# Kernel tuning notes

Hardware: AMD Instinct MI355X
Metric: run time of the kernel (lower is better)

## Reference

```python
import jax, jax.numpy as jnp
import numpy as np

D_MODEL = 1024
NHEAD = 16
NUM_KV = 4
D_K = D_MODEL // NHEAD          # 64
GROUP = NHEAD // NUM_KV          # 4 query heads per kv head
ROPE_BASE = 10000.0


def _rope(x, seq_len):
    """Apply rotary embedding. x: [B, h, S, d_k], positions 0..seq_len-1."""
    half = D_K // 2
    inv_freq = 1.0 / (ROPE_BASE ** (jnp.arange(0, D_K, 2, dtype=jnp.float32) / D_K))
    t = jnp.arange(seq_len, dtype=jnp.float32)
    freqs = jnp.outer(t, inv_freq)                      # [S, d_k/2]
    emb = jnp.concatenate([freqs, freqs], axis=-1)      # [S, d_k]
    cos, sin = jnp.cos(emb), jnp.sin(emb)               # broadcast over B, h
    x1, x2 = x[..., :half], x[..., half:]
    rot = jnp.concatenate([-x2, x1], axis=-1)
    return x * cos + rot * sin


def setup_inputs() -> dict:
    key = jax.random.key(0)
    ks = jax.random.split(key, 12)
    B, S = 2, 2048
    s_in = 1.0 / np.sqrt(D_MODEL)
    inp = {
        "query": jax.random.normal(ks[0], (B, S, D_MODEL), jnp.float32),
        "key":   jax.random.normal(ks[1], (B, S, D_MODEL), jnp.float32),
        "value": jax.random.normal(ks[2], (B, S, D_MODEL), jnp.float32),
        "Wq": jax.random.normal(ks[3], (D_MODEL, D_MODEL), jnp.float32) * s_in,
        "bq": jnp.zeros((D_MODEL,), jnp.float32),
        "Wk": jax.random.normal(ks[4], (NUM_KV * D_K, D_MODEL), jnp.float32) * s_in,
        "bk": jnp.zeros((NUM_KV * D_K,), jnp.float32),
        "Wv": jax.random.normal(ks[5], (NUM_KV * D_K, D_MODEL), jnp.float32) * s_in,
        "bv": jnp.zeros((NUM_KV * D_K,), jnp.float32),
        "Wo": jax.random.normal(ks[6], (D_MODEL, D_MODEL), jnp.float32) * s_in,
        "bo": jnp.zeros((D_MODEL,), jnp.float32),
    }
    return inp


def reference(query, key, value, Wq, bq, Wk, bk, Wv, bv, Wo, bo):
    B, S, _ = query.shape
    T = key.shape[1]
    # projections (torch Linear: x @ W^T + b)
    Q = (query @ Wq.T + bq).reshape(B, S, NHEAD, D_K).transpose(0, 2, 1, 3)   # [B,H,S,dk]
    K = (key   @ Wk.T + bk).reshape(B, T, NUM_KV, D_K).transpose(0, 2, 1, 3)  # [B,KV,T,dk]
    V = (value @ Wv.T + bv).reshape(B, T, NUM_KV, D_K).transpose(0, 2, 1, 3)
    # fused RoPE (start_pos = 0)
    Q = _rope(Q, S)
    K = _rope(K, T)
    # expand kv heads (repeat_interleave on head dim)
    Kr = jnp.repeat(K, GROUP, axis=1)   # [B,H,T,dk]
    Vr = jnp.repeat(V, GROUP, axis=1)
    scale = 1.0 / np.sqrt(D_K)
    scores = jnp.einsum("bhsd,bhtd->bhst", Q, Kr) * scale   # [B,H,S,T]
    attn = jax.nn.softmax(scores, axis=-1)                    # dropout = eval/no-op
    context = jnp.einsum("bhst,bhtd->bhsd", attn, Vr)        # [B,H,S,dk]
    context = context.transpose(0, 2, 1, 3).reshape(B, S, D_MODEL)
    return context @ Wo.T + bo
```

## Files before the change

kernel.cpp:

```cpp
#include <hip/hip_runtime.h>
#include <hip/hip_bf16.h>

typedef __hip_bfloat16 bf16;
typedef __attribute__((ext_vector_type(8))) short short8;
typedef __attribute__((ext_vector_type(4))) short short4v;
typedef __attribute__((ext_vector_type(4))) float f32x4;
typedef __attribute__((ext_vector_type(4))) float float4v;

static __device__ inline short f2bf(float f){
  __hip_bfloat16 h = __float2bfloat16(f);
  return *reinterpret_cast<short*>(&h);
}

static __device__ __forceinline__ unsigned cvt_pk_bf16(float lo, float hi){
  unsigned r;
  asm("v_cvt_pk_bf16_f32 %0, %1, %2" : "=v"(r) : "v"(lo), "v"(hi));
  return r;
}

static __device__ __forceinline__ float exp2_fast(float x){
  float r;
  asm("v_exp_f32 %0, %1" : "=v"(r) : "v"(x));
  return r;
}

static __device__ __forceinline__ float max3f(float a, float b, float c){
  float r;
  asm("v_max3_f32 %0, %1, %2, %3" : "=v"(r) : "v"(a), "v"(b), "v"(c));
  return r;
}

static __device__ inline short8 load8(const float* p){
  float4v a = *reinterpret_cast<const float4v*>(p);
  float4v b = *reinterpret_cast<const float4v*>(p + 4);
  short8 r;
  unsigned* u = reinterpret_cast<unsigned*>(&r);
  u[0] = cvt_pk_bf16(a[0], a[1]);
  u[1] = cvt_pk_bf16(a[2], a[3]);
  u[2] = cvt_pk_bf16(b[0], b[1]);
  u[3] = cvt_pk_bf16(b[2], b[3]);
  return r;
}
static __device__ inline short8 load8(const bf16* p){
  return *reinterpret_cast<const short8*>(p);
}

typedef __attribute__((address_space(1))) const unsigned int gas_u32;
typedef __attribute__((address_space(3))) unsigned int las_u32;
static __device__ __forceinline__ void gload16(const void* g, void* l){
  __builtin_amdgcn_global_load_lds((gas_u32*)g, (las_u32*)l, 16, 0, 0);
}

template<int N>
static __device__ __forceinline__ void vm_barrier(){
  if constexpr (N == 8) asm volatile("s_waitcnt vmcnt(8)" ::: "memory");
  else if constexpr (N == 4) asm volatile("s_waitcnt vmcnt(4)" ::: "memory");
  else if constexpr (N == 2) asm volatile("s_waitcnt vmcnt(2)" ::: "memory");
  else asm volatile("s_waitcnt vmcnt(0)" ::: "memory");
  __builtin_amdgcn_s_barrier();
  __builtin_amdgcn_sched_barrier(0);
}

#define CVT_Q   0
#define CVT_K   4194304
#define CVT_V   8388608
#define CVT_WQ  12582912
#define CVT_WK  13631488
#define CVT_WV  13893632
#define CVT_WO  14155776
#define CVT_TOT 15204352
__global__ void cvt_kernel(bf16* __restrict__ dst, float* __restrict__ tab,
    const float* q, const float* k, const float* v,
    const float* wq, const float* wk, const float* wv, const float* wo){
  if (blockIdx.x < 256){
    const int idx = blockIdx.x * 256 + threadIdx.x;
    const int d = idx & 31, s = idx >> 5;
    const float ang = (float)s * exp2f(-0.41524101186092030f * (float)d);
    float sn, cs;
    sincosf(ang, &sn, &cs);
    tab[idx*2] = cs; tab[idx*2+1] = sn;
  }
  const size_t i8 = ((size_t)blockIdx.x * 256 + threadIdx.x) * 8;
  const float* src; size_t off;
  if      (i8 < CVT_K ){ src = q;  off = i8; }
  else if (i8 < CVT_V ){ src = k;  off = i8 - CVT_K; }
  else if (i8 < CVT_WQ){ src = v;  off = i8 - CVT_V; }
  else if (i8 < CVT_WK){ src = wq; off = i8 - CVT_WQ; }
  else if (i8 < CVT_WV){ src = wk; off = i8 - CVT_WK; }
  else if (i8 < CVT_WO){ src = wv; off = i8 - CVT_WV; }
  else                 { src = wo; off = i8 - CVT_WO; }
  *reinterpret_cast<short8*>(reinterpret_cast<short*>(dst) + i8) = load8(src + off);
}

template<int MODE>
__device__ __forceinline__ void gemm_bt_v2(
    short* lds, void* __restrict__ Cout,
    const bf16* __restrict__ A, const bf16* __restrict__ B,
    const float* __restrict__ bias, const float* __restrict__ tab,
    int ntile, int mtile, int N, int K)
{
  const int NK = K >> 5;
  const int n0 = ntile * 128, m0 = mtile * 128;
  const int tid = threadIdx.x, w = tid >> 6, lane = tid & 63;
  const int wm = w >> 1, wn = w & 1, lr = lane & 15, lg = lane >> 4;
  const int r0 = w*32 + (lane >> 2), r1 = r0 + 16;
  const int c0 = ((lane & 3) ^ ((r0 >> 1) & 3)) * 8;
  const int c1 = ((lane & 3) ^ ((r1 >> 1) & 3)) * 8;
  const bf16* A0 = A + (size_t)(m0 + r0) * K + c0;
  const bf16* A1 = A + (size_t)(m0 + r1) * K + c1;
  const bf16* B0 = B + (size_t)(n0 + r0) * K + c0;
  const bf16* B1 = B + (size_t)(n0 + r1) * K + c1;
  const int ldsW = (w*32) * 32;
  int offA[4], offB[4];
  #pragma unroll
  for (int i = 0; i < 4; i++){
    const int ra = wm*64 + i*16 + lr;
    offA[i] = ra*64 + ((lg ^ ((ra >> 1) & 3)) * 16);
    const int rb = wn*64 + i*16 + lr;
    offB[i] = rb*64 + ((lg ^ ((rb >> 1) & 3)) * 16);
  }
  auto stage = [&](int t){
    short* bufA = lds + (t & 3) * 8192;
    short* bufB = bufA + 4096;
    gload16(A0 + t*32, bufA + ldsW);
    gload16(A1 + t*32, bufA + ldsW + 512);
    gload16(B0 + t*32, bufB + ldsW);
    gload16(B1 + t*32, bufB + ldsW + 512);
  };
  f32x4 acc[4][4] = {};
  stage(0); stage(1);
  for (int t = 0; t < NK; t++){
    if (t + 2 < NK){ stage(t + 2); vm_barrier<8>(); }
    else if (t + 1 < NK){ vm_barrier<4>(); }
    else { vm_barrier<0>(); }
    const char* bufA = (const char*)(lds + (t & 3) * 8192);
    const char* bufB = bufA + 8192;
    short8 af[4], bfm[4];
    #pragma unroll
    for (int mt = 0; mt < 4; mt++) af[mt]  = *(const short8*)(bufA + offA[mt]);
    #pragma unroll
    for (int nt = 0; nt < 4; nt++) bfm[nt] = *(const short8*)(bufB + offB[nt]);
    __builtin_amdgcn_s_setprio(1);
    #pragma unroll
    for (int mt = 0; mt < 4; mt++)
      #pragma unroll
      for (int nt = 0; nt < 4; nt++)
        acc[mt][nt] = __builtin_amdgcn_mfma_f32_16x16x32_bf16(af[mt], bfm[nt], acc[mt][nt], 0, 0, 0);
    __builtin_amdgcn_s_setprio(0);
  }
  if constexpr (MODE == 0){
    float* C = (float*)Cout;
    #pragma unroll
    for (int mt = 0; mt < 4; mt++){
      #pragma unroll
      for (int nt = 0; nt < 4; nt++){
        const int col = n0 + wn*64 + nt*16 + lr;
        const float bv = bias[col];
        const int rbase = m0 + wm*64 + mt*16 + lg*4;
        #pragma unroll
        for (int i = 0; i < 4; i++)
          C[(size_t)(rbase + i) * N + col] = acc[mt][nt][i] + bv;
      }
    }
  } else if constexpr (MODE == 1 || MODE == 2){
    bf16* dst = (bf16*)Cout;
    constexpr int NH = (MODE == 1) ? 16 : 4;
    constexpr float SC = (MODE == 1) ? 0.18033688011112042f : 1.0f;
    #pragma unroll
    for (int mt = 0; mt < 4; mt++){
      #pragma unroll
      for (int nt = 0; nt < 2; nt++){
        const int col = n0 + wn*64 + nt*16 + lr;
        const int d = col & 63;
        const int hh = col >> 6;
        const float b1 = bias[col], b2 = bias[col + 32];
        #pragma unroll
        for (int i = 0; i < 4; i++){
          const int m = m0 + wm*64 + mt*16 + lg*4 + i;
          const int s = m & 2047, bb = m >> 11;
          const float cs = tab[(s*32 + d)*2], sn = tab[(s*32 + d)*2 + 1];
          const float x1 = acc[mt][nt][i] + b1;
          const float x2 = acc[mt][nt+2][i] + b2;
          const size_t o = ((size_t)(bb*NH + hh) * 2048 + s) * 64 + d;
          dst[o]      = __float2bfloat16((x1*cs - x2*sn) * SC);
          dst[o + 32] = __float2bfloat16((x2*cs + x1*sn) * SC);
        }
      }
    }
  } else {
    bf16* dst = (bf16*)Cout;
    #pragma unroll
    for (int mt = 0; mt < 4; mt++){
      #pragma unroll
      for (int nt = 0; nt < 4; nt++){
        const int col = n0 + wn*64 + nt*16 + lr;
        const int kv = col >> 6, d = col & 63;
        const float bv = bias[col];
        #pragma unroll
        for (int i = 0; i < 4; i++){
          const int m = m0 + wm*64 + mt*16 + lg*4 + i;
          const int s = m & 2047, bb = m >> 11;
          dst[((size_t)(bb*4 + kv) * 64 + d) * 2048 + s] = __float2bfloat16(acc[mt][nt][i] + bv);
        }
      }
    }
  }
}

__global__ __launch_bounds__(256, 2) void gemm_qkv_kernel(
    bf16* Qa, bf16* Ka, bf16* Va, const bf16* cvt,
    const float* bq, const float* bk, const float* bv, const float* tab){
  __shared__ short lds[4 * 8192];
  const int pid = blockIdx.x;
  const int x = pid >> 5;
  const int y = (pid & 7) * 4 + ((pid >> 3) & 3);
  if (x < 8)
    gemm_bt_v2<1>(lds, Qa, cvt + CVT_Q, cvt + CVT_WQ, bq, tab, x,    y, 1024, 1024);
  else if (x < 10)
    gemm_bt_v2<2>(lds, Ka, cvt + CVT_K, cvt + CVT_WK, bk, tab, x-8,  y, 256, 1024);
  else
    gemm_bt_v2<3>(lds, Va, cvt + CVT_V, cvt + CVT_WV, bv, tab, x-10, y, 256, 1024);
}
__global__ __launch_bounds__(256, 2) void gemm_out_kernel(
    float* C, const bf16* ctx, const bf16* cvt, const float* bo){
  __shared__ short lds[4 * 8192];
  const int pid = blockIdx.x;
  const int x = pid >> 5;
  const int y = (pid & 7) * 4 + ((pid >> 3) & 3);
  gemm_bt_v2<0>(lds, C, ctx, cvt + CVT_WO, bo, nullptr, x, y, 1024, 1024);
}

__global__ __launch_bounds__(256, 2) void attn_kernel(
    bf16* __restrict__ ctx, const bf16* __restrict__ Qa,
    const bf16* __restrict__ Ka, const bf16* __restrict__ Vt)
{
  __shared__ short Klds[4][64 * 64];
  __shared__ short Vlds[4][64 * 64];
  const int pid = blockIdx.y * 16 + blockIdx.x;
  const int bh = (pid & 7) * 4 + ((pid >> 3) & 3);
  const int q0 = (pid >> 5) * 128;
  const int b = bh >> 4, h = bh & 15, kvh = h >> 2;
  const int tid = threadIdx.x, w = tid >> 6, lane = tid & 63;
  const int lr = lane & 15, lg = lane >> 4;
  const bf16* Qbase = Qa + (size_t)bh * 2048 * 64;
  const bf16* Kbase = Ka + (size_t)(b*4 + kvh) * 2048 * 64;
  const bf16* Vbase = Vt + (size_t)(b*4 + kvh) * 64 * 2048;

  short8 qf[2][2];
  #pragma unroll
  for (int qt = 0; qt < 2; qt++){
    qf[qt][0] = load8(Qbase + (size_t)(q0 + w*32 + qt*16 + lr) * 64 + lg*8);
    qf[qt][1] = load8(Qbase + (size_t)(q0 + w*32 + qt*16 + lr) * 64 + 32 + lg*8);
  }

  const int xsw = (lr & 7) << 4;
  const int koff0 = lr*128 + ((lg*16) ^ xsw);
  const int koff1 = lr*128 + ((64 + lg*16) ^ xsw);
  int voff[2][2];
  #pragma unroll
  for (int kkA = 0; kkA < 2; kkA++)
    #pragma unroll
    for (int hh = 0; hh < 2; hh++)
      voff[kkA][hh] = lr*128 + ((kkA*64 + lg*8 + hh*32) ^ xsw);

  const int l8 = lane >> 3;
  const int ch = (lane & 7) ^ l8;
  const bf16* kSrc = Kbase + (size_t)(w*16 + l8) * 64 + ch*8;
  const bf16* vSrc = Vbase + (size_t)(w*16 + l8) * 2048 + ch*8;
  auto stage = [&](int bi, int t){
    short* Kd = &Klds[bi][(w*16) * 64];
    short* Vd = &Vlds[bi][(w*16) * 64];
    const bf16* ks = kSrc + (size_t)t * 64 * 64;
    const bf16* vs = vSrc + t * 64;
    gload16(ks,           Kd);
    gload16(ks + 8*64,    Kd + 8*64);
    gload16(vs,           Vd);
    gload16(vs + 8*2048,  Vd + 8*64);
  };

  float mrow[2] = {-1e30f, -1e30f};
  f32x4 o[2][4] = {};
  f32x4 acc_l[2] = {};
  short8 ones;
  #pragma unroll
  for (int j = 0; j < 4; j++) reinterpret_cast<unsigned*>(&ones)[j] = 0x3F803F80u;

  auto qk = [&](const char* Kc, f32x4 (&st)[4][2]){
    __builtin_amdgcn_s_setprio(1);
    #pragma unroll
    for (int mt = 0; mt < 4; mt++){
      short8 kf0 = *reinterpret_cast<const short8*>(Kc + mt*2048 + koff0);
      short8 kf1 = *reinterpret_cast<const short8*>(Kc + mt*2048 + koff1);
      #pragma unroll
      for (int qt = 0; qt < 2; qt++){
        st[mt][qt] = __builtin_amdgcn_mfma_f32_16x16x32_bf16(kf0, qf[qt][0], (f32x4){0.f,0.f,0.f,0.f}, 0, 0, 0);
        st[mt][qt] = __builtin_amdgcn_mfma_f32_16x16x32_bf16(kf1, qf[qt][1], st[mt][qt], 0, 0, 0);
      }
    }
    __builtin_amdgcn_s_setprio(0);
  };

  auto softmax_pv = [&](f32x4 (&st)[4][2], const char* Vc){
    short8 pf[2][2];
    #pragma unroll
    for (int qt = 0; qt < 2; qt++){
      const float m0 = max3f(st[0][qt][0], st[0][qt][1], st[0][qt][2]);
      const float m1 = max3f(st[0][qt][3], st[1][qt][0], st[1][qt][1]);
      const float m2 = max3f(st[1][qt][2], st[1][qt][3], st[2][qt][0]);
      const float m3 = max3f(st[2][qt][1], st[2][qt][2], st[2][qt][3]);
      const float m4 = max3f(st[3][qt][0], st[3][qt][1], st[3][qt][2]);
      float mx = fmaxf(max3f(m0, m1, m2), max3f(m3, m4, st[3][qt][3]));
      if (__any(mx > mrow[qt] + 8.0f)){
        mx = fmaxf(mx, __shfl_xor(mx, 16));
        mx = fmaxf(mx, __shfl_xor(mx, 32));
        const float nm = fmaxf(mrow[qt], mx);
        const float alpha = exp2_fast(mrow[qt] - nm);
        mrow[qt] = nm;
        float ab[4];
        #pragma unroll
        for (int i = 0; i < 4; i++) ab[i] = __shfl(alpha, lg*4 + i);
        #pragma unroll
        for (int dt = 0; dt < 4; dt++)
          #pragma unroll
          for (int i = 0; i < 4; i++)
            o[qt][dt][i] *= ab[i];
        #pragma unroll
        for (int i = 0; i < 4; i++) acc_l[qt][i] *= ab[i];
      }
      unsigned* pw = reinterpret_cast<unsigned*>(&pf[qt][0]);
      #pragma unroll
      for (int j = 0; j < 8; j++){
        const int mt = j >> 1, i0 = (j & 1) * 2;
        const float e0 = exp2_fast(st[mt][qt][i0]     - mrow[qt]);
        const float e1 = exp2_fast(st[mt][qt][i0 + 1] - mrow[qt]);
        pw[j] = cvt_pk_bf16(e0, e1);
      }
    }
    __builtin_amdgcn_s_setprio(1);
    #pragma unroll
    for (int qt = 0; qt < 2; qt++){
      acc_l[qt] = __builtin_amdgcn_mfma_f32_16x16x32_bf16(pf[qt][0], ones, acc_l[qt], 0, 0, 0);
      acc_l[qt] = __builtin_amdgcn_mfma_f32_16x16x32_bf16(pf[qt][1], ones, acc_l[qt], 0, 0, 0);
    }
    #pragma unroll
    for (int dt = 0; dt < 4; dt++){
      #pragma unroll
      for (int kkA = 0; kkA < 2; kkA++){
        short8 vf;
        *reinterpret_cast<short4v*>(&vf) =
            *reinterpret_cast<const short4v*>(Vc + dt*2048 + voff[kkA][0]);
        *reinterpret_cast<short4v*>(reinterpret_cast<short*>(&vf) + 4) =
            *reinterpret_cast<const short4v*>(Vc + dt*2048 + voff[kkA][1]);
        #pragma unroll
        for (int qt = 0; qt < 2; qt++)
          o[qt][dt] = __builtin_amdgcn_mfma_f32_16x16x32_bf16(pf[qt][kkA], vf, o[qt][dt], 0, 0, 0);
      }
    }
    __builtin_amdgcn_s_setprio(0);
  };

  f32x4 stA[4][2], stB[4][2];

  stage(0, 0); stage(1, 1);
  vm_barrier<4>();
  qk((const char*)&Klds[0][0], stA);

  for (int tt = 0; tt < 32; tt += 2){
    if (tt + 2 < 32){ stage((tt+2) & 3, tt+2); vm_barrier<4>(); }
    else vm_barrier<0>();
    qk((const char*)&Klds[(tt+1) & 3][0], stB);
    softmax_pv(stA, (const char*)&Vlds[tt & 3][0]);
    if (tt + 3 < 32){ stage((tt+3) & 3, tt+3); vm_barrier<4>(); }
    else vm_barrier<0>();
    if (tt + 2 < 32) qk((const char*)&Klds[(tt+2) & 3][0], stA);
    softmax_pv(stB, (const char*)&Vlds[(tt+1) & 3][0]);
  }

  #pragma unroll
  for (int qt = 0; qt < 2; qt++){
    float lb[4];
    #pragma unroll
    for (int i = 0; i < 4; i++) lb[i] = 1.0f / acc_l[qt][i];
    #pragma unroll
    for (int dt = 0; dt < 4; dt++){
      #pragma unroll
      for (int i = 0; i < 4; i++){
        const int q = q0 + w*32 + qt*16 + lg*4 + i;
        ctx[(size_t)(b*2048 + q) * 1024 + h*64 + dt*16 + lr] =
            __float2bfloat16(o[qt][dt][i] * lb[i]);
      }
    }
  }
}

extern "C" void kernel_launch(void* const* d_in, const int* in_sizes, int n_in,
                              void* d_out, int out_size, void* d_ws, size_t ws_size,
                              hipStream_t stream)
{
  const float* query = (const float*)d_in[0];
  const float* key   = (const float*)d_in[1];
  const float* value = (const float*)d_in[2];
  const float* Wq = (const float*)d_in[3];
  const float* bq = (const float*)d_in[4];
  const float* Wk = (const float*)d_in[5];
  const float* bk = (const float*)d_in[6];
  const float* Wv = (const float*)d_in[7];
  const float* bv = (const float*)d_in[8];
  const float* Wo = (const float*)d_in[9];
  const float* bo = (const float*)d_in[10];
  float* out = (float*)d_out;

  char* ws = (char*)d_ws;
  size_t off = 0;
  float* tab = (float*)(ws + off); off += (size_t)2048 * 32 * 2 * 4;
  bf16*  Qa  = (bf16*)(ws + off);  off += (size_t)32 * 2048 * 64 * 2;
  bf16*  Ka  = (bf16*)(ws + off);  off += (size_t)8 * 2048 * 64 * 2;
  bf16*  Va  = (bf16*)(ws + off);  off += (size_t)8 * 64 * 2048 * 2;
  bf16*  ctx = (bf16*)(ws + off);  off += (size_t)2 * 2048 * 1024 * 2;
  bf16*  cvt = (bf16*)(ws + off);  off += (size_t)CVT_TOT * 2;

  cvt_kernel<<<CVT_TOT / 8 / 256, 256, 0, stream>>>(cvt, tab, query, key, value, Wq, Wk, Wv, Wo);
  gemm_qkv_kernel<<<384, 256, 0, stream>>>(Qa, Ka, Va, cvt, bq, bk, bv, tab);
  attn_kernel<<<dim3(16, 32), 256, 0, stream>>>(ctx, Qa, Ka, Va);
  gemm_out_kernel<<<256, 256, 0, stream>>>(out, ctx, cvt, bo);
}
```

Measured before the change: 104.2 us.

## Use 128-key attention tiles with double-buffered LDS and a simple loop

The attention kernel now processes 128 keys per iteration instead of 64. It uses two LDS buffers with a new XOR-swizzled V layout, in place of a four-deep ring. The software-pipelined schedule that overlapped the next tile's QK with the current tile's softmax/PV is removed in favour of a straight loop: prefetch the next tile, compute, then barrier. This halves loop iterations and barrier count and amortises softmax bookkeeping over larger tiles. In exchange it gives up the intra-wave overlap of QK and softmax/PV and doubles the score registers held per wave, which may reduce latency hiding.

After: 100.4 us (median of 2 runs). 3.6% less time.

```diff
diff --git a/kernel.cpp b/kernel.cpp
--- a/kernel.cpp
+++ b/kernel.cpp
@@ -234,8 +234,8 @@
     bf16* __restrict__ ctx, const bf16* __restrict__ Qa,
     const bf16* __restrict__ Ka, const bf16* __restrict__ Vt)
 {
-  __shared__ short Klds[4][64 * 64];
-  __shared__ short Vlds[4][64 * 64];
+  __shared__ short Klds[2][128 * 64];
+  __shared__ short Vlds[2][64 * 128];
   const int pid = blockIdx.y * 16 + blockIdx.x;
   const int bh = (pid & 7) * 4 + ((pid >> 3) & 3);
   const int q0 = (pid >> 5) * 128;
@@ -253,29 +253,33 @@
     qf[qt][1] = load8(Qbase + (size_t)(q0 + w*32 + qt*16 + lr) * 64 + 32 + lg*8);
   }
 
-  const int xsw = (lr & 7) << 4;
-  const int koff0 = lr*128 + ((lg*16) ^ xsw);
-  const int koff1 = lr*128 + ((64 + lg*16) ^ xsw);
-  int voff[2][2];
-  #pragma unroll
-  for (int kkA = 0; kkA < 2; kkA++)
+  const int xswk = (lr & 7) << 4;
+  const int koff0 = lr*128 + ((lg*16) ^ xswk);
+  const int koff1 = lr*128 + ((64 + lg*16) ^ xswk);
+  int voff[4][2];
+  #pragma unroll
+  for (int kkA = 0; kkA < 4; kkA++)
     #pragma unroll
     for (int hh = 0; hh < 2; hh++)
-      voff[kkA][hh] = lr*128 + ((kkA*64 + lg*8 + hh*32) ^ xsw);
+      voff[kkA][hh] = lr*256 + (((kkA*4 + hh*2 + (lg >> 1)) ^ lr) << 4) + (lg & 1)*8;
 
   const int l8 = lane >> 3;
-  const int ch = (lane & 7) ^ l8;
-  const bf16* kSrc = Kbase + (size_t)(w*16 + l8) * 64 + ch*8;
-  const bf16* vSrc = Vbase + (size_t)(w*16 + l8) * 2048 + ch*8;
+  const int chk = (lane & 7) ^ l8;
+  const bf16* kSrc = Kbase + (size_t)(w*32 + l8) * 64 + chk*8;
+  const int vr0 = lane >> 4;
+  const bf16* vSrc[4];
+  #pragma unroll
+  for (int j = 0; j < 4; j++)
+    vSrc[j] = Vbase + (size_t)(w*16 + j*4 + vr0) * 2048 + ((lane & 15) ^ (j*4 + vr0)) * 8;
+
   auto stage = [&](int bi, int t){
-    short* Kd = &Klds[bi][(w*16) * 64];
-    short* Vd = &Vlds[bi][(w*16) * 64];
-    const bf16* ks = kSrc + (size_t)t * 64 * 64;
-    const bf16* vs = vSrc + t * 64;
-    gload16(ks,           Kd);
-    gload16(ks + 8*64,    Kd + 8*64);
-    gload16(vs,           Vd);
-    gload16(vs + 8*2048,  Vd + 8*64);
+    short* Kd = &Klds[bi][(w*32) * 64];
+    short* Vd = &Vlds[bi][(w*16) * 128];
+    const bf16* ks = kSrc + (size_t)t * 8192;
+    #pragma unroll
+    for (int j = 0; j < 4; j++) gload16(ks + j*512, Kd + j*512);
+    #pragma unroll
+    for (int j = 0; j < 4; j++) gload16(vSrc[j] + t*128, Vd + j*512);
   };
 
   float mrow[2] = {-1e30f, -1e30f};
@@ -285,10 +289,18 @@
   #pragma unroll
   for (int j = 0; j < 4; j++) reinterpret_cast<unsigned*>(&ones)[j] = 0x3F803F80u;
 
-  auto qk = [&](const char* Kc, f32x4 (&st)[4][2]){
+  f32x4 st[8][2];
+
+  stage(0, 0);
+  vm_barrier<0>();
+
+  for (int t = 0; t < 16; t++){
+    if (t + 1 < 16) stage((t+1) & 1, t+1);
+
+    const char* Kc = (const char*)&Klds[t & 1][0];
     __builtin_amdgcn_s_setprio(1);
     #pragma unroll
-    for (int mt = 0; mt < 4; mt++){
+    for (int mt = 0; mt < 8; mt++){
       short8 kf0 = *reinterpret_cast<const short8*>(Kc + mt*2048 + koff0);
       short8 kf1 = *reinterpret_cast<const short8*>(Kc + mt*2048 + koff1);
       #pragma unroll
@@ -298,18 +310,18 @@
       }
     }
     __builtin_amdgcn_s_setprio(0);
-  };
-
-  auto softmax_pv = [&](f32x4 (&st)[4][2], const char* Vc){
-    short8 pf[2][2];
+
+    short8 pf[2][4];
     #pragma unroll
     for (int qt = 0; qt < 2; qt++){
-      const float m0 = max3f(st[0][qt][0], st[0][qt][1], st[0][qt][2]);
-      const float m1 = max3f(st[0][qt][3], st[1][qt][0], st[1][qt][1]);
-      const float m2 = max3f(st[1][qt][2], st[1][qt][3], st[2][qt][0]);
-      const float m3 = max3f(st[2][qt][1], st[2][qt][2], st[2][qt][3]);
-      const float m4 = max3f(st[3][qt][0], st[3][qt][1], st[3][qt][2]);
-      float mx = fmaxf(max3f(m0, m1, m2), max3f(m3, m4, st[3][qt][3]));
+      float m8[8];
+      #pragma unroll
+      for (int mt = 0; mt < 8; mt++)
+        m8[mt] = fmaxf(max3f(st[mt][qt][0], st[mt][qt][1], st[mt][qt][2]), st[mt][qt][3]);
+      const float a  = max3f(m8[0], m8[1], m8[2]);
+      const float bb = max3f(m8[3], m8[4], m8[5]);
+      const float c  = max3f(m8[6], m8[7], a);
+      float mx = fmaxf(bb, c);
       if (__any(mx > mrow[qt] + 8.0f)){
         mx = fmaxf(mx, __shfl_xor(mx, 16));
         mx = fmaxf(mx, __shfl_xor(mx, 32));
@@ -329,51 +341,38 @@
       }
       unsigned* pw = reinterpret_cast<unsigned*>(&pf[qt][0]);
       #pragma unroll
-      for (int j = 0; j < 8; j++){
-        const int mt = j >> 1, i0 = (j & 1) * 2;
+      for (int p = 0; p < 16; p++){
+        const int mt = p >> 1, i0 = (p & 1) * 2;
         const float e0 = exp2_fast(st[mt][qt][i0]     - mrow[qt]);
         const float e1 = exp2_fast(st[mt][qt][i0 + 1] - mrow[qt]);
-        pw[j] = cvt_pk_bf16(e0, e1);
-      }
-    }
+        pw[p] = cvt_pk_bf16(e0, e1);
+      }
+    }
+
+    const char* Vc = (const char*)&Vlds[t & 1][0];
     __builtin_amdgcn_s_setprio(1);
     #pragma unroll
-    for (int qt = 0; qt < 2; qt++){
-      acc_l[qt] = __builtin_amdgcn_mfma_f32_16x16x32_bf16(pf[qt][0], ones, acc_l[qt], 0, 0, 0);
-      acc_l[qt] = __builtin_amdgcn_mfma_f32_16x16x32_bf16(pf[qt][1], ones, acc_l[qt], 0, 0, 0);
-    }
+    for (int qt = 0; qt < 2; qt++)
+      #pragma unroll
+      for (int kkA = 0; kkA < 4; kkA++)
+        acc_l[qt] = __builtin_amdgcn_mfma_f32_16x16x32_bf16(pf[qt][kkA], ones, acc_l[qt], 0, 0, 0);
     #pragma unroll
     for (int dt = 0; dt < 4; dt++){
       #pragma unroll
-      for (int kkA = 0; kkA < 2; kkA++){
+      for (int kkA = 0; kkA < 4; kkA++){
         short8 vf;
         *reinterpret_cast<short4v*>(&vf) =
-            *reinterpret_cast<const short4v*>(Vc + dt*2048 + voff[kkA][0]);
+            *reinterpret_cast<const short4v*>(Vc + dt*4096 + voff[kkA][0]);
         *reinterpret_cast<short4v*>(reinterpret_cast<short*>(&vf) + 4) =
-            *reinterpret_cast<const short4v*>(Vc + dt*2048 + voff[kkA][1]);
+            *reinterpret_cast<const short4v*>(Vc + dt*4096 + voff[kkA][1]);
         #pragma unroll
         for (int qt = 0; qt < 2; qt++)
           o[qt][dt] = __builtin_amdgcn_mfma_f32_16x16x32_bf16(pf[qt][kkA], vf, o[qt][dt], 0, 0, 0);
       }
     }
     __builtin_amdgcn_s_setprio(0);
-  };
-
-  f32x4 stA[4][2], stB[4][2];
-
-  stage(0, 0); stage(1, 1);
-  vm_barrier<4>();
-  qk((const char*)&Klds[0][0], stA);
-
-  for (int tt = 0; tt < 32; tt += 2){
-    if (tt + 2 < 32){ stage((tt+2) & 3, tt+2); vm_barrier<4>(); }
-    else vm_barrier<0>();
-    qk((const char*)&Klds[(tt+1) & 3][0], stB);
-    softmax_pv(stA, (const char*)&Vlds[tt & 3][0]);
-    if (tt + 3 < 32){ stage((tt+3) & 3, tt+3); vm_barrier<4>(); }
-    else vm_barrier<0>();
-    if (tt + 2 < 32) qk((const char*)&Klds[(tt+2) & 3][0], stA);
-    softmax_pv(stB, (const char*)&Vlds[(tt+1) & 3][0]);
+
+    if (t + 1 < 16) vm_barrier<0>();
   }
 
   #pragma unroll
```

## Split attention KV range across warps with LDS merge of partial softmax

Applied to the files above, without the earlier changes.

The attention kernel now gives each block 32 queries instead of 128, and each of its 4 warps walks a separate quarter of the 2048 keys. Every warp keeps its own private LDS slice with single-buffered staging. At the end the warps write their partial outputs, row maxima and row sums to LDS and merge them flash-decoding style. The grid grows from 512 to 2048 blocks to raise parallelism and occupancy, at the cost of 4x more Q-side block overhead, extra K/V global reads per query, and a final LDS reduction.

Measured after the change: 128.5 us, median of 2. 23.3% more time.

```diff
diff --git a/kernel.cpp b/kernel.cpp
--- a/kernel.cpp
+++ b/kernel.cpp
@@ -234,48 +234,48 @@
     bf16* __restrict__ ctx, const bf16* __restrict__ Qa,
     const bf16* __restrict__ Ka, const bf16* __restrict__ Vt)
 {
-  __shared__ short Klds[4][64 * 64];
-  __shared__ short Vlds[4][64 * 64];
-  const int pid = blockIdx.y * 16 + blockIdx.x;
+  __shared__ char lds[4][16384];
+  const int pid = blockIdx.x;
   const int bh = (pid & 7) * 4 + ((pid >> 3) & 3);
-  const int q0 = (pid >> 5) * 128;
+  const int q0 = (pid >> 5) * 32;
   const int b = bh >> 4, h = bh & 15, kvh = h >> 2;
   const int tid = threadIdx.x, w = tid >> 6, lane = tid & 63;
   const int lr = lane & 15, lg = lane >> 4;
   const bf16* Qbase = Qa + (size_t)bh * 2048 * 64;
   const bf16* Kbase = Ka + (size_t)(b*4 + kvh) * 2048 * 64;
   const bf16* Vbase = Vt + (size_t)(b*4 + kvh) * 64 * 2048;
+  char* Kc = lds[w];
+  char* Vc = lds[w] + 8192;
+  const int kv0 = w * 512;
 
   short8 qf[2][2];
   #pragma unroll
   for (int qt = 0; qt < 2; qt++){
-    qf[qt][0] = load8(Qbase + (size_t)(q0 + w*32 + qt*16 + lr) * 64 + lg*8);
-    qf[qt][1] = load8(Qbase + (size_t)(q0 + w*32 + qt*16 + lr) * 64 + 32 + lg*8);
-  }
-
-  const int xsw = (lr & 7) << 4;
-  const int koff0 = lr*128 + ((lg*16) ^ xsw);
-  const int koff1 = lr*128 + ((64 + lg*16) ^ xsw);
+    qf[qt][0] = load8(Qbase + (size_t)(q0 + qt*16 + lr) * 64 + lg*8);
+    qf[qt][1] = load8(Qbase + (size_t)(q0 + qt*16 + lr) * 64 + 32 + lg*8);
+  }
+
+  const int xs = lr & 7;
+  const int koff0 = lr*128 + ((lg       ^ xs) << 4);
+  const int koff1 = lr*128 + (((4 + lg) ^ xs) << 4);
   int voff[2][2];
   #pragma unroll
   for (int kkA = 0; kkA < 2; kkA++)
     #pragma unroll
     for (int hh = 0; hh < 2; hh++)
-      voff[kkA][hh] = lr*128 + ((kkA*64 + lg*8 + hh*32) ^ xsw);
+      voff[kkA][hh] = lr*128 + (((kkA*4 + hh*2 + (lg >> 1)) ^ xs) << 4) + (lg & 1)*8;
 
   const int l8 = lane >> 3;
   const int ch = (lane & 7) ^ l8;
-  const bf16* kSrc = Kbase + (size_t)(w*16 + l8) * 64 + ch*8;
-  const bf16* vSrc = Vbase + (size_t)(w*16 + l8) * 2048 + ch*8;
-  auto stage = [&](int bi, int t){
-    short* Kd = &Klds[bi][(w*16) * 64];
-    short* Vd = &Vlds[bi][(w*16) * 64];
-    const bf16* ks = kSrc + (size_t)t * 64 * 64;
-    const bf16* vs = vSrc + t * 64;
-    gload16(ks,           Kd);
-    gload16(ks + 8*64,    Kd + 8*64);
-    gload16(vs,           Vd);
-    gload16(vs + 8*2048,  Vd + 8*64);
+  const bf16* kS = Kbase + (size_t)(kv0 + l8) * 64 + ch*8;
+  const bf16* vS = Vbase + (size_t)l8 * 2048 + kv0 + ch*8;
+  auto stage = [&](int t){
+    const bf16* ks = kS + (size_t)t * 4096;
+    #pragma unroll
+    for (int jj = 0; jj < 8; jj++) gload16(ks + jj*512, Kc + jj*1024);
+    const bf16* vs = vS + t * 64;
+    #pragma unroll
+    for (int jj = 0; jj < 8; jj++) gload16(vs + (size_t)jj*16384, Vc + jj*1024);
   };
 
   float mrow[2] = {-1e30f, -1e30f};
@@ -285,7 +285,12 @@
   #pragma unroll
   for (int j = 0; j < 4; j++) reinterpret_cast<unsigned*>(&ones)[j] = 0x3F803F80u;
 
-  auto qk = [&](const char* Kc, f32x4 (&st)[4][2]){
+  stage(0);
+  asm volatile("s_waitcnt vmcnt(0)" ::: "memory");
+  __builtin_amdgcn_sched_barrier(0);
+
+  for (int t = 0; t < 8; t++){
+    f32x4 st[4][2];
     __builtin_amdgcn_s_setprio(1);
     #pragma unroll
     for (int mt = 0; mt < 4; mt++){
@@ -298,9 +303,21 @@
       }
     }
     __builtin_amdgcn_s_setprio(0);
-  };
-
-  auto softmax_pv = [&](f32x4 (&st)[4][2], const char* Vc){
+
+    short8 vf[4][2];
+    #pragma unroll
+    for (int dt = 0; dt < 4; dt++)
+      #pragma unroll
+      for (int kkA = 0; kkA < 2; kkA++){
+        *reinterpret_cast<short4v*>(&vf[dt][kkA]) =
+            *reinterpret_cast<const short4v*>(Vc + dt*2048 + voff[kkA][0]);
+        *reinterpret_cast<short4v*>(reinterpret_cast<short*>(&vf[dt][kkA]) + 4) =
+            *reinterpret_cast<const short4v*>(Vc + dt*2048 + voff[kkA][1]);
+      }
+    asm volatile("s_waitcnt lgkmcnt(0)" ::: "memory");
+    __builtin_amdgcn_sched_barrier(0);
+    if (t + 1 < 8) stage(t + 1);
+
     short8 pf[2][2];
     #pragma unroll
     for (int qt = 0; qt < 2; qt++){
@@ -336,6 +353,7 @@
         pw[j] = cvt_pk_bf16(e0, e1);
       }
     }
+
     __builtin_amdgcn_s_setprio(1);
     #pragma unroll
     for (int qt = 0; qt < 2; qt++){
@@ -343,51 +361,68 @@
       acc_l[qt] = __builtin_amdgcn_mfma_f32_16x16x32_bf16(pf[qt][1], ones, acc_l[qt], 0, 0, 0);
     }
     #pragma unroll
+    for (int dt = 0; dt < 4; dt++)
+      #pragma unroll
+      for (int kkA = 0; kkA < 2; kkA++)
+        #pragma unroll
+        for (int qt = 0; qt < 2; qt++)
+          o[qt][dt] = __builtin_amdgcn_mfma_f32_16x16x32_bf16(pf[qt][kkA], vf[dt][kkA], o[qt][dt], 0, 0, 0);
+    __builtin_amdgcn_s_setprio(0);
+
+    if (t + 1 < 8){
+      asm volatile("s_waitcnt vmcnt(0)" ::: "memory");
+      __builtin_amdgcn_sched_barrier(0);
+    }
+  }
+
+  float* Wf = (float*)lds[w];
+  #pragma unroll
+  for (int qt = 0; qt < 2; qt++){
+    #pragma unroll
+    for (int dt = 0; dt < 4; dt++)
+      #pragma unroll
+      for (int i = 0; i < 4; i++)
+        Wf[(qt*16 + lg*4 + i)*64 + dt*16 + lr] = o[qt][dt][i];
+    #pragma unroll
+    for (int i = 0; i < 4; i++){
+      const float mq = __shfl(mrow[qt], lg*4 + i);
+      if (lr == 0){
+        Wf[2048 + qt*32 + (lg*4 + i)*2]     = mq;
+        Wf[2048 + qt*32 + (lg*4 + i)*2 + 1] = acc_l[qt][i];
+      }
+    }
+  }
+  asm volatile("s_waitcnt lgkmcnt(0)" ::: "memory");
+  __builtin_amdgcn_s_barrier();
+  __builtin_amdgcn_sched_barrier(0);
+
+  #pragma unroll
+  for (int qt = 0; qt < 2; qt++){
+    float lbi[4], sc0[4], sc1[4], sc2[4], sc3[4];
+    #pragma unroll
+    for (int i = 0; i < 4; i++){
+      const int slot = 2048 + qt*32 + (lg*4 + i)*2;
+      const float mw0 = ((const float*)lds[0])[slot], lw0 = ((const float*)lds[0])[slot+1];
+      const float mw1 = ((const float*)lds[1])[slot], lw1 = ((const float*)lds[1])[slot+1];
+      const float mw2 = ((const float*)lds[2])[slot], lw2 = ((const float*)lds[2])[slot+1];
+      const float mw3 = ((const float*)lds[3])[slot], lw3 = ((const float*)lds[3])[slot+1];
+      const float M = fmaxf(max3f(mw0, mw1, mw2), mw3);
+      sc0[i] = exp2_fast(mw0 - M); sc1[i] = exp2_fast(mw1 - M);
+      sc2[i] = exp2_fast(mw2 - M); sc3[i] = exp2_fast(mw3 - M);
+      lbi[i] = 1.0f / (lw0*sc0[i] + lw1*sc1[i] + lw2*sc2[i] + lw3*sc3[i]);
+    }
+    #pragma unroll
     for (int dt = 0; dt < 4; dt++){
       #pragma unroll
-      for (int kkA = 0; kkA < 2; kkA++){
-        short8 vf;
-        *reinterpret_cast<short4v*>(&vf) =
-            *reinterpret_cast<const short4v*>(Vc + dt*2048 + voff[kkA][0]);
-        *reinterpret_cast<short4v*>(reinterpret_cast<short*>(&vf) + 4) =
-            *reinterpret_cast<const short4v*>(Vc + dt*2048 + voff[kkA][1]);
-        #pragma unroll
-        for (int qt = 0; qt < 2; qt++)
-          o[qt][dt] = __builtin_amdgcn_mfma_f32_16x16x32_bf16(pf[qt][kkA], vf, o[qt][dt], 0, 0, 0);
-      }
-    }
-    __builtin_amdgcn_s_setprio(0);
-  };
-
-  f32x4 stA[4][2], stB[4][2];
-
-  stage(0, 0); stage(1, 1);
-  vm_barrier<4>();
-  qk((const char*)&Klds[0][0], stA);
-
-  for (int tt = 0; tt < 32; tt += 2){
-    if (tt + 2 < 32){ stage((tt+2) & 3, tt+2); vm_barrier<4>(); }
-    else vm_barrier<0>();
-    qk((const char*)&Klds[(tt+1) & 3][0], stB);
-    softmax_pv(stA, (const char*)&Vlds[tt & 3][0]);
-    if (tt + 3 < 32){ stage((tt+3) & 3, tt+3); vm_barrier<4>(); }
-    else vm_barrier<0>();
-    if (tt + 2 < 32) qk((const char*)&Klds[(tt+2) & 3][0], stA);
-    softmax_pv(stB, (const char*)&Vlds[(tt+1) & 3][0]);
-  }
-
-  #pragma unroll
-  for (int qt = 0; qt < 2; qt++){
-    float lb[4];
-    #pragma unroll
-    for (int i = 0; i < 4; i++) lb[i] = 1.0f / acc_l[qt][i];
-    #pragma unroll
-    for (int dt = 0; dt < 4; dt++){
-      #pragma unroll
       for (int i = 0; i < 4; i++){
-        const int q = q0 + w*32 + qt*16 + lg*4 + i;
+        const int idx = (qt*16 + lg*4 + i)*64 + dt*16 + lr;
+        const float om = ((const float*)lds[0])[idx]*sc0[i]
+                       + ((const float*)lds[1])[idx]*sc1[i]
+                       + ((const float*)lds[2])[idx]*sc2[i]
+                       + ((const float*)lds[3])[idx]*sc3[i];
+        const int q = q0 + qt*16 + lg*4 + i;
         ctx[(size_t)(b*2048 + q) * 1024 + h*64 + dt*16 + lr] =
-            __float2bfloat16(o[qt][dt][i] * lb[i]);
+            __float2bfloat16(om * lbi[i]);
       }
     }
   }
@@ -421,6 +456,6 @@
 
   cvt_kernel<<<CVT_TOT / 8 / 256, 256, 0, stream>>>(cvt, tab, query, key, value, Wq, Wk, Wv, Wo);
   gemm_qkv_kernel<<<384, 256, 0, stream>>>(Qa, Ka, Va, cvt, bq, bk, bv, tab);
-  attn_kernel<<<dim3(16, 32), 256, 0, stream>>>(ctx, Qa, Ka, Va);
+  attn_kernel<<<2048, 256, 0, stream>>>(ctx, Qa, Ka, Va);
   gemm_out_kernel<<<256, 256, 0, stream>>>(out, ctx, cvt, bo);
 }
```
